# Kernel optimization log

Measured on AMD Instinct MI355X. Metric: run time of the kernel, lower is better.

Reference implementation:

```python
import jax, jax.numpy as jnp
import numpy as np

NUM_CLASSES = 19
EPS = 1e-8  # torch cosine_similarity eps


def setup_inputs() -> dict:
    key = jax.random.key(0)
    k1, k2 = jax.random.split(key)
    inputs = jax.random.normal(k1, (8, 64, 512, 512), dtype=jnp.float32)
    targets = jax.random.randint(k2, (8, 512, 512), 0, NUM_CLASSES, dtype=jnp.int64)
    return {"inputs": inputs, "targets": targets}


def reference(inputs, targets):
    K = NUM_CLASSES
    B, C, H, W = inputs.shape
    # Flatten pixels: [N, C] features, [N] labels
    x = inputs.transpose(0, 2, 3, 1).reshape(-1, C)
    t = targets.reshape(-1)
    # Per-class centroids via one scatter-sum (replaces the per-class mask loop)
    sums = jax.ops.segment_sum(x, t, num_segments=K)  # [K, C]
    counts = jax.ops.segment_sum(jnp.ones_like(t, dtype=x.dtype), t, num_segments=K)  # [K]
    centers = sums / jnp.maximum(counts, 1.0)[:, None]  # [K, C]
    # Pairwise cosine similarity (torch clamps each norm by eps)
    norms = jnp.maximum(jnp.sqrt(jnp.sum(centers * centers, axis=1)), EPS)
    cn = centers / norms[:, None]
    S = cn @ cn.T  # [K, K] cosine sim matrix
    # CosineEmbeddingLoss: y=+1 (diag) -> 1 - cos; y=-1 -> max(0, cos).
    # Original: sum_i mean_j loss_ij, then / K^2  ==  sum_ij loss_ij / K^3
    eye = jnp.eye(K, dtype=bool)
    per_pair = jnp.where(eye, 1.0 - S, jnp.maximum(S, 0.0))
    return jnp.sum(per_pair) / (K * K * K)
```

## Files before the change

kernel.cpp:

```cpp
#include <hip/hip_runtime.h>

#define NK 19
#define NC 64
#define HW (512*512)
#define BLOCK 256
#define PPB 1024
#define NTILES 16
#define TPIX 64
#define TROW 66
#define NBLOCKS 2048
#define SUMS (NK*NC)
#define MAXCOPIES 64

__global__ __launch_bounds__(BLOCK) void accum_kernel(
    const float* __restrict__ x, const int* __restrict__ t,
    float* __restrict__ ws, int copymask) {
  __shared__ float tile[NC * TROW];
  __shared__ int   lbl[PPB];
  __shared__ float bins[4][SUMS];

  const int tid = threadIdx.x;
  const int bid = blockIdx.x;
  const int batch   = bid >> 8;
  const int pixbase = (bid & 255) << 10;

  {
    const int4 l4 = *reinterpret_cast<const int4*>(
        t + (size_t)batch * HW + pixbase + tid * 4);
    *reinterpret_cast<int4*>(&lbl[tid * 4]) = l4;
  }

  const int r = tid >> 2, s = tid & 3;
  const float* xrow = x + (size_t)(batch * NC + r) * HW + pixbase;
  float* tdst = &tile[r * TROW + s * 4];

  const int wv = tid >> 6, ln = tid & 63;
  const int cb = ln & 15, pg = ln >> 4;

  float acc[NK][4];
#pragma unroll
  for (int k = 0; k < NK; ++k) {
#pragma unroll
    for (int j = 0; j < 4; ++j) acc[k][j] = 0.0f;
  }

  for (int tl = 0; tl < NTILES; ++tl) {
    const float* src = xrow + tl * TPIX + s * 4;
    const float4 a0 = *reinterpret_cast<const float4*>(src + 0);
    const float4 a1 = *reinterpret_cast<const float4*>(src + 16);
    const float4 a2 = *reinterpret_cast<const float4*>(src + 32);
    const float4 a3 = *reinterpret_cast<const float4*>(src + 48);
    __syncthreads();
    *reinterpret_cast<float4*>(tdst + 0)  = a0;
    *reinterpret_cast<float4*>(tdst + 16) = a1;
    *reinterpret_cast<float4*>(tdst + 32) = a2;
    *reinterpret_cast<float4*>(tdst + 48) = a3;
    __syncthreads();

    const int pb = wv * 16;
#pragma unroll
    for (int i = 0; i < 4; ++i) {
      const int p = pb + i * 4 + pg;
      const int lab = lbl[tl * TPIX + p];
      const float v0 = tile[(cb +  0) * TROW + p];
      const float v1 = tile[(cb + 16) * TROW + p];
      const float v2 = tile[(cb + 32) * TROW + p];
      const float v3 = tile[(cb + 48) * TROW + p];
#pragma unroll
      for (int k = 0; k < NK; ++k) {
        const float sel = (lab == k) ? 1.0f : 0.0f;
        acc[k][0] = fmaf(v0, sel, acc[k][0]);
        acc[k][1] = fmaf(v1, sel, acc[k][1]);
        acc[k][2] = fmaf(v2, sel, acc[k][2]);
        acc[k][3] = fmaf(v3, sel, acc[k][3]);
      }
    }
  }

#pragma unroll
  for (int k = 0; k < NK; ++k) {
#pragma unroll
    for (int j = 0; j < 4; ++j) {
      float v = acc[k][j];
      v += __shfl_xor(v, 16, 64);
      v += __shfl_xor(v, 32, 64);
      acc[k][j] = v;
    }
  }
  if (pg == 0) {
#pragma unroll
    for (int k = 0; k < NK; ++k) {
#pragma unroll
      for (int j = 0; j < 4; ++j)
        bins[wv][k * NC + cb + 16 * j] = acc[k][j];
    }
  }
  __syncthreads();

  float* base = ws + (size_t)(bid & copymask) * SUMS;
  for (int i = tid; i < SUMS; i += BLOCK) {
    float v = bins[0][i] + bins[1][i] + bins[2][i] + bins[3][i];
    unsafeAtomicAdd(base + i, v);
  }
}

__global__ __launch_bounds__(BLOCK) void hist_kernel(
    const int* __restrict__ t, float* __restrict__ cnts) {
  int cnt[NK];
#pragma unroll
  for (int k = 0; k < NK; ++k) cnt[k] = 0;
  const int tid = threadIdx.x;
  const size_t base = (size_t)blockIdx.x * 8192;
#pragma unroll
  for (int q = 0; q < 8; ++q) {
    const int4 l4 = *reinterpret_cast<const int4*>(t + base + q * 1024 + tid * 4);
#pragma unroll
    for (int k = 0; k < NK; ++k)
      cnt[k] += (l4.x == k) + (l4.y == k) + (l4.z == k) + (l4.w == k);
  }
#pragma unroll
  for (int k = 0; k < NK; ++k) {
    int v = cnt[k];
    v += __shfl_xor(v, 1, 64);  v += __shfl_xor(v, 2, 64);
    v += __shfl_xor(v, 4, 64);  v += __shfl_xor(v, 8, 64);
    v += __shfl_xor(v, 16, 64); v += __shfl_xor(v, 32, 64);
    cnt[k] = v;
  }
  if ((tid & 63) == 0) {
#pragma unroll
    for (int k = 0; k < NK; ++k)
      unsafeAtomicAdd(cnts + k, (float)cnt[k]);
  }
}

__global__ __launch_bounds__(512) void finalize_kernel(
    const float* __restrict__ ws, const float* __restrict__ cnts,
    float* __restrict__ out, int ncopies) {
  __shared__ float cen[SUMS];
  __shared__ float invn[NK];
  __shared__ float cc[NK];
  __shared__ float red[8];

  const int tid = threadIdx.x;
  if (tid < NK) cc[tid] = fmaxf(cnts[tid], 1.0f);
  __syncthreads();

  for (int i = tid; i < SUMS; i += 512) {
    float s = 0.0f;
    for (int r = 0; r < ncopies; ++r) s += ws[(size_t)r * SUMS + i];
    cen[i] = s / cc[i >> 6];
  }
  __syncthreads();

  if (tid < NK) {
    float sq = 0.0f;
    for (int c = 0; c < NC; ++c) { float v = cen[tid * NC + c]; sq += v * v; }
    invn[tid] = 1.0f / fmaxf(sqrtf(sq), 1e-8f);
  }
  __syncthreads();

  float contrib = 0.0f;
  if (tid < NK * NK) {
    int i = tid / NK, j = tid - (tid / NK) * NK;
    float dot = 0.0f;
    for (int c = 0; c < NC; ++c) dot += cen[i * NC + c] * cen[j * NC + c];
    float S = dot * invn[i] * invn[j];
    contrib = (i == j) ? (1.0f - S) : fmaxf(S, 0.0f);
  }
  for (int off = 32; off > 0; off >>= 1) contrib += __shfl_down(contrib, off, 64);
  if ((tid & 63) == 0) red[tid >> 6] = contrib;
  __syncthreads();
  if (tid == 0) {
    float s = 0.0f;
    for (int w = 0; w < 8; ++w) s += red[w];
    out[0] = s / 6859.0f;
  }
}

extern "C" void kernel_launch(void* const* d_in, const int* in_sizes, int n_in,
                              void* d_out, int out_size, void* d_ws, size_t ws_size,
                              hipStream_t stream) {
  const float* x = (const float*)d_in[0];
  const int*   t = (const int*)d_in[1];
  float* ws = (float*)d_ws;

  int ncopies = 1;
  while (ncopies < MAXCOPIES &&
         (size_t)(ncopies * 2 * SUMS + 32) * sizeof(float) <= ws_size)
    ncopies *= 2;
  float* cnts = ws + (size_t)ncopies * SUMS;

  hipMemsetAsync(d_ws, 0, ((size_t)ncopies * SUMS + 32) * sizeof(float), stream);
  accum_kernel<<<NBLOCKS, BLOCK, 0, stream>>>(x, t, ws, ncopies - 1);
  hist_kernel<<<256, BLOCK, 0, stream>>>(t, cnts);
  finalize_kernel<<<1, 512, 0, stream>>>(ws, cnts, (float*)d_out, ncopies);
}
```

Before: 991.3 us.

## Stream channel groups per wave directly from global, drop LDS tiling

Each wave now owns four channels of one batch image and reads float4 pixel vectors and labels directly from global memory, removing the shared-memory transpose tile and block-level barriers. Partial sums are reduced with full-wave shuffles and written with per-wave global atomics instead of a block-level LDS reduction. This trades away the LDS traffic and synchronization for redundant label reads (once per channel group) and more atomics and shuffle work.

```diff
diff --git a/kernel.cpp b/kernel.cpp
--- a/kernel.cpp
+++ b/kernel.cpp
@@ -4,103 +4,84 @@
 #define NC 64
 #define HW (512*512)
 #define BLOCK 256
-#define PPB 1024
-#define NTILES 16
-#define TPIX 64
-#define TROW 66
 #define NBLOCKS 2048
 #define SUMS (NK*NC)
 #define MAXCOPIES 64
+#define CHUNKS 16
+#define CPX 256
 
-__global__ __launch_bounds__(BLOCK) void accum_kernel(
+__global__ __launch_bounds__(BLOCK, 4) void accum_kernel(
     const float* __restrict__ x, const int* __restrict__ t,
     float* __restrict__ ws, int copymask) {
-  __shared__ float tile[NC * TROW];
-  __shared__ int   lbl[PPB];
-  __shared__ float bins[4][SUMS];
+  const int tid = threadIdx.x;
+  const int wv = tid >> 6, ln = tid & 63;
+  const int wid   = (blockIdx.x << 2) + wv;
+  const int combo = wid >> 6;
+  const int batch = combo >> 4;
+  const int c0    = (combo & 15) << 2;
+  const int sub   = wid & 63;
+  const size_t pix0 = (size_t)sub * (CHUNKS * CPX);
 
-  const int tid = threadIdx.x;
-  const int bid = blockIdx.x;
-  const int batch   = bid >> 8;
-  const int pixbase = (bid & 255) << 10;
-
-  {
-    const int4 l4 = *reinterpret_cast<const int4*>(
-        t + (size_t)batch * HW + pixbase + tid * 4);
-    *reinterpret_cast<int4*>(&lbl[tid * 4]) = l4;
-  }
-
-  const int r = tid >> 2, s = tid & 3;
-  const float* xrow = x + (size_t)(batch * NC + r) * HW + pixbase;
-  float* tdst = &tile[r * TROW + s * 4];
-
-  const int wv = tid >> 6, ln = tid & 63;
-  const int cb = ln & 15, pg = ln >> 4;
+  const float* xr0 = x + (size_t)(batch * NC + c0) * HW + pix0 + (ln << 2);
+  const float* xr1 = xr0 + HW;
+  const float* xr2 = xr1 + HW;
+  const float* xr3 = xr2 + HW;
+  const int*   tr  = t + (size_t)batch * HW + pix0 + (ln << 2);
 
   float acc[NK][4];
 #pragma unroll
-  for (int k = 0; k < NK; ++k) {
+  for (int k = 0; k < NK; ++k)
 #pragma unroll
     for (int j = 0; j < 4; ++j) acc[k][j] = 0.0f;
-  }
 
-  for (int tl = 0; tl < NTILES; ++tl) {
-    const float* src = xrow + tl * TPIX + s * 4;
-    const float4 a0 = *reinterpret_cast<const float4*>(src + 0);
-    const float4 a1 = *reinterpret_cast<const float4*>(src + 16);
-    const float4 a2 = *reinterpret_cast<const float4*>(src + 32);
-    const float4 a3 = *reinterpret_cast<const float4*>(src + 48);
-    __syncthreads();
-    *reinterpret_cast<float4*>(tdst + 0)  = a0;
-    *reinterpret_cast<float4*>(tdst + 16) = a1;
-    *reinterpret_cast<float4*>(tdst + 32) = a2;
-    *reinterpret_cast<float4*>(tdst + 48) = a3;
-    __syncthreads();
-
-    const int pb = wv * 16;
+#pragma unroll 1
+  for (int ch = 0; ch < CHUNKS; ++ch) {
+    const int off = ch * CPX;
+    const float4 v0 = *reinterpret_cast<const float4*>(xr0 + off);
+    const float4 v1 = *reinterpret_cast<const float4*>(xr1 + off);
+    const float4 v2 = *reinterpret_cast<const float4*>(xr2 + off);
+    const float4 v3 = *reinterpret_cast<const float4*>(xr3 + off);
+    const int4   lb = *reinterpret_cast<const int4*>(tr + off);
+    const float a0[4] = {v0.x, v0.y, v0.z, v0.w};
+    const float a1[4] = {v1.x, v1.y, v1.z, v1.w};
+    const float a2[4] = {v2.x, v2.y, v2.z, v2.w};
+    const float a3[4] = {v3.x, v3.y, v3.z, v3.w};
+    const int  lbs[4] = {lb.x, lb.y, lb.z, lb.w};
 #pragma unroll
-    for (int i = 0; i < 4; ++i) {
-      const int p = pb + i * 4 + pg;
-      const int lab = lbl[tl * TPIX + p];
-      const float v0 = tile[(cb +  0) * TROW + p];
-      const float v1 = tile[(cb + 16) * TROW + p];
-      const float v2 = tile[(cb + 32) * TROW + p];
-      const float v3 = tile[(cb + 48) * TROW + p];
+    for (int q = 0; q < 4; ++q) {
+      const int lab = lbs[q];
+      const float f0 = a0[q], f1 = a1[q], f2 = a2[q], f3 = a3[q];
 #pragma unroll
       for (int k = 0; k < NK; ++k) {
         const float sel = (lab == k) ? 1.0f : 0.0f;
-        acc[k][0] = fmaf(v0, sel, acc[k][0]);
-        acc[k][1] = fmaf(v1, sel, acc[k][1]);
-        acc[k][2] = fmaf(v2, sel, acc[k][2]);
-        acc[k][3] = fmaf(v3, sel, acc[k][3]);
+        acc[k][0] = fmaf(f0, sel, acc[k][0]);
+        acc[k][1] = fmaf(f1, sel, acc[k][1]);
+        acc[k][2] = fmaf(f2, sel, acc[k][2]);
+        acc[k][3] = fmaf(f3, sel, acc[k][3]);
       }
     }
   }
 
 #pragma unroll
-  for (int k = 0; k < NK; ++k) {
+  for (int k = 0; k < NK; ++k)
 #pragma unroll
     for (int j = 0; j < 4; ++j) {
       float v = acc[k][j];
-      v += __shfl_xor(v, 16, 64);
-      v += __shfl_xor(v, 32, 64);
+      v += __shfl_xor(v, 1, 64);  v += __shfl_xor(v, 2, 64);
+      v += __shfl_xor(v, 4, 64);  v += __shfl_xor(v, 8, 64);
+      v += __shfl_xor(v, 16, 64); v += __shfl_xor(v, 32, 64);
       acc[k][j] = v;
     }
-  }
-  if (pg == 0) {
+
+  if (ln == 0) {
+    float* base = ws + (size_t)(wid & copymask) * SUMS + c0;
 #pragma unroll
     for (int k = 0; k < NK; ++k) {
-#pragma unroll
-      for (int j = 0; j < 4; ++j)
-        bins[wv][k * NC + cb + 16 * j] = acc[k][j];
+      unsafeAtomicAdd(base + k * NC + 0, acc[k][0]);
+      unsafeAtomicAdd(base + k * NC + 1, acc[k][1]);
+      unsafeAtomicAdd(base + k * NC + 2, acc[k][2]);
+      unsafeAtomicAdd(base + k * NC + 3, acc[k][3]);
     }
-  }
-  __syncthreads();
-
-  float* base = ws + (size_t)(bid & copymask) * SUMS;
-  for (int i = tid; i < SUMS; i += BLOCK) {
-    float v = bins[0][i] + bins[1][i] + bins[2][i] + bins[3][i];
-    unsafeAtomicAdd(base + i, v);
   }
 }
 
```

Result: no change. 1.002 ms (+1.1%).
